# Performance work log

Hardware: AMD Instinct MI355X
Metric: run time of the kernel (lower is better)

The kernel has to match this reference:

```python
import jax, jax.numpy as jnp
import numpy as np

V, E, H, T = 50000, 512, 256, 32  # vocab, embed dim, per-direction hidden, tagset
START, STOP = 30, 31
S = 2048  # sequence length
NEG = -10000.0


def setup_inputs() -> dict:
    key = jax.random.key(0)
    ks = jax.random.split(key, 16)
    sentence = jax.random.randint(ks[0], (S,), 0, V)
    embed = jax.random.normal(ks[1], (V, E), dtype=jnp.float32)
    # PyTorch LSTM layout: gates stacked [i, f, g, o], each H rows
    w_ih_f = jax.random.normal(ks[2], (4 * H, E), dtype=jnp.float32) * 0.05
    w_hh_f = jax.random.normal(ks[3], (4 * H, H), dtype=jnp.float32) * 0.05
    b_f = jax.random.normal(ks[4], (4 * H,), dtype=jnp.float32) * 0.05  # b_ih + b_hh fused
    w_ih_b = jax.random.normal(ks[5], (4 * H, E), dtype=jnp.float32) * 0.05
    w_hh_b = jax.random.normal(ks[6], (4 * H, H), dtype=jnp.float32) * 0.05
    b_b = jax.random.normal(ks[7], (4 * H,), dtype=jnp.float32) * 0.05
    w_tag = jax.random.normal(ks[8], (T, 2 * H), dtype=jnp.float32) * 0.05
    b_tag = jax.random.normal(ks[9], (T,), dtype=jnp.float32) * 0.05
    transitions = jax.random.normal(ks[10], (T, T), dtype=jnp.float32)
    transitions = transitions.at[START, :].set(NEG)  # nothing transitions into START
    transitions = transitions.at[:, STOP].set(NEG)   # nothing transitions out of STOP
    h0 = jax.random.normal(ks[11], (2, H), dtype=jnp.float32)  # [fwd/bwd, H]
    c0 = jax.random.normal(ks[12], (2, H), dtype=jnp.float32)
    return {"sentence": sentence, "embed": embed, "w_ih_f": w_ih_f, "w_hh_f": w_hh_f,
            "b_f": b_f, "w_ih_b": w_ih_b, "w_hh_b": w_hh_b, "b_b": b_b,
            "w_tag": w_tag, "b_tag": b_tag, "transitions": transitions,
            "h0": h0, "c0": c0}


def _run_lstm(x, w_ih, w_hh, b, h, c):
    # x: [S, E]; precompute input projections for all steps at once
    px = x @ w_ih.T + b  # [S, 4H]

    def step(carry, p):
        h, c = carry
        g = p + h @ w_hh.T  # [4H]
        i, f, gg, o = jnp.split(g, 4)
        c = jax.nn.sigmoid(f) * c + jax.nn.sigmoid(i) * jnp.tanh(gg)
        h = jax.nn.sigmoid(o) * jnp.tanh(c)
        return (h, c), h

    _, hs = jax.lax.scan(step, (h, c), px)
    return hs  # [S, H]


def _lstm_features(sentence, embed, w_ih_f, w_hh_f, b_f, w_ih_b, w_hh_b, b_b,
                   w_tag, b_tag, h0, c0):
    emb = embed[sentence]  # [S, E]
    h_fwd = _run_lstm(emb, w_ih_f, w_hh_f, b_f, h0[0], c0[0])
    h_bwd = _run_lstm(emb[::-1], w_ih_b, w_hh_b, b_b, h0[1], c0[1])[::-1]
    hs = jnp.concatenate([h_fwd, h_bwd], axis=-1)  # [S, 2H]
    return hs @ w_tag.T + b_tag  # [S, T]


def _viterbi(feats, transitions):
    init = jnp.full((T,), NEG, dtype=feats.dtype).at[START].set(0.0)

    def step(fv, feat):
        scores = fv[None, :] + transitions  # [next_tag, prev_tag]
        bptrs = jnp.argmax(scores, axis=1)  # [T]
        fv_new = jnp.max(scores, axis=1) + feat
        return fv_new, bptrs

    fv, bptrs = jax.lax.scan(step, init, feats)  # bptrs: [S, T]
    terminal = fv + transitions[STOP]
    best_last = jnp.argmax(terminal)
    path_score = terminal[best_last]

    def back(tag, bp):
        return bp[tag], tag

    _, tag_seq = jax.lax.scan(back, best_last, bptrs, reverse=True)  # [S]
    return path_score, tag_seq


def reference(sentence, embed, w_ih_f, w_hh_f, b_f, w_ih_b, w_hh_b, b_b,
              w_tag, b_tag, transitions, h0, c0):
    feats = _lstm_features(sentence, embed, w_ih_f, w_hh_f, b_f,
                           w_ih_b, w_hh_b, b_b, w_tag, b_tag, h0, c0)
    score, tag_seq = _viterbi(feats, transitions)
    return score, tag_seq
```

## Files before the change

kernel.cpp:

```cpp
#include <hip/hip_runtime.h>
#include <cstdint>
#include <cmath>

constexpr int SEQ  = 2048;
constexpr int EMB  = 512;
constexpr int HID  = 256;
constexpr int GATE = 1024;
constexpr int NTAG = 32;
constexpr float FNEG = -10000.0f;
constexpr int DBLK = 8;

__global__ __launch_bounds__(256) void px_gemm(
    const int* __restrict__ sent, const float* __restrict__ embed,
    const float* __restrict__ w_ih_f, const float* __restrict__ b_f,
    const float* __restrict__ w_ih_b, const float* __restrict__ b_b,
    float* __restrict__ px)
{
  const int dir = blockIdx.z;
  const int tm = blockIdx.x, tn = blockIdx.y;
  const float* __restrict__ w_ih = dir ? w_ih_b : w_ih_f;
  const float* __restrict__ bias = dir ? b_b : b_f;
  __shared__ float As[64][65];
  __shared__ float Bs[64][65];
  __shared__ int sidx[64];
  const int tid = threadIdx.x;
  if (tid < 64) {
    const int s = tm * 64 + tid;
    const int tpos = dir ? (SEQ - 1 - s) : s;
    sidx[tid] = sent[tpos];
  }
  __syncthreads();
  float acc[4][4] = {};
  const int tr = tid >> 4, tc = tid & 15;
  for (int k0 = 0; k0 < EMB; k0 += 64) {
    #pragma unroll
    for (int i = 0; i < 4; ++i) {
      const int v = tid + i * 256;
      const int r = v >> 4, kv = v & 15;
      const float4 a4 = *reinterpret_cast<const float4*>(
          &embed[(size_t)sidx[r] * EMB + k0 + kv * 4]);
      As[r][kv*4+0] = a4.x; As[r][kv*4+1] = a4.y;
      As[r][kv*4+2] = a4.z; As[r][kv*4+3] = a4.w;
      const float4 b4 = *reinterpret_cast<const float4*>(
          &w_ih[(size_t)(tn * 64 + r) * EMB + k0 + kv * 4]);
      Bs[r][kv*4+0] = b4.x; Bs[r][kv*4+1] = b4.y;
      Bs[r][kv*4+2] = b4.z; Bs[r][kv*4+3] = b4.w;
    }
    __syncthreads();
    #pragma unroll
    for (int kk = 0; kk < 64; ++kk) {
      float a[4], b[4];
      #pragma unroll
      for (int i = 0; i < 4; ++i) a[i] = As[tr + 16 * i][kk];
      #pragma unroll
      for (int jj = 0; jj < 4; ++jj) b[jj] = Bs[tc + 16 * jj][kk];
      #pragma unroll
      for (int i = 0; i < 4; ++i)
        #pragma unroll
        for (int jj = 0; jj < 4; ++jj)
          acc[i][jj] = fmaf(a[i], b[jj], acc[i][jj]);
    }
    __syncthreads();
  }
  #pragma unroll
  for (int i = 0; i < 4; ++i) {
    const int srow = tm * 64 + tr + 16 * i;
    #pragma unroll
    for (int jj = 0; jj < 4; ++jj) {
      const int j = tn * 64 + tc + 16 * jj;
      px[((size_t)dir * SEQ + srow) * GATE + j] = acc[i][jj] + bias[j];
    }
  }
}

__global__ __attribute__((amdgpu_flat_work_group_size(256, 256),
                          amdgpu_waves_per_eu(1, 1)))
void lstm_sync(
    const float* __restrict__ px, const float* __restrict__ w_hh_f,
    const float* __restrict__ w_hh_b, const float* __restrict__ h0,
    const float* __restrict__ c0, float* __restrict__ hs,
    unsigned long long* __restrict__ hx)
{
  const int blk = blockIdx.x;
  const int dir = blk >> 3, b = blk & 7;
  const int tid = threadIdx.x;
  const int j = tid >> 3;
  const int q = tid & 7;
  const int u = 32 * b + j;
  const float* __restrict__ w_hh = dir ? w_hh_b : w_hh_f;

  float4 wi[8], wf[8], wg[8], wo[8];
  {
    const float* __restrict__ r0 = &w_hh[(size_t)u * HID + 32 * q];
    const float* __restrict__ r1 = r0 + (size_t)256 * HID;
    const float* __restrict__ r2 = r0 + (size_t)512 * HID;
    const float* __restrict__ r3 = r0 + (size_t)768 * HID;
    #pragma unroll
    for (int m = 0; m < 8; ++m) {
      wi[m] = *reinterpret_cast<const float4*>(&r0[4 * m]);
      wf[m] = *reinterpret_cast<const float4*>(&r1[4 * m]);
      wg[m] = *reinterpret_cast<const float4*>(&r2[4 * m]);
      wo[m] = *reinterpret_cast<const float4*>(&r3[4 * m]);
    }
  }
  #pragma unroll
  for (int m = 0; m < 8; ++m) {
    asm volatile(""
      : "+v"(wi[m].x), "+v"(wi[m].y), "+v"(wi[m].z), "+v"(wi[m].w),
        "+v"(wf[m].x), "+v"(wf[m].y), "+v"(wf[m].z), "+v"(wf[m].w),
        "+v"(wg[m].x), "+v"(wg[m].y), "+v"(wg[m].z), "+v"(wg[m].w),
        "+v"(wo[m].x), "+v"(wo[m].y), "+v"(wo[m].z), "+v"(wo[m].w));
  }

  __shared__ float hsh[2][8 * 36];
  float c = 0.0f;
  hsh[0][36 * (tid >> 5) + (tid & 31)] = h0[dir * HID + tid];
  if (q == 0) c = c0[dir * HID + u];
  __syncthreads();

  const size_t pxbase = (size_t)dir * SEQ * GATE;
  float pi = 0.f, pf = 0.f, pg = 0.f, po = 0.f;
  if (q == 0) {
    pi = px[pxbase + u];        pf = px[pxbase + 256 + u];
    pg = px[pxbase + 512 + u];  po = px[pxbase + 768 + u];
  }

  for (int t = 0; t < SEQ; ++t) {
    const float* __restrict__ hb = hsh[t & 1];
    float*       __restrict__ nb = hsh[(t & 1) ^ 1];

    float ni = 0.f, nf = 0.f, ng = 0.f, no = 0.f;
    if (q == 0 && t + 1 < SEQ) {
      const size_t nbx = pxbase + (size_t)(t + 1) * GATE;
      ni = px[nbx + u];        nf = px[nbx + 256 + u];
      ng = px[nbx + 512 + u];  no = px[nbx + 768 + u];
    }

    float si = 0.f, sf = 0.f, sg = 0.f, so = 0.f;
    #pragma unroll
    for (int m = 0; m < 8; ++m) {
      const float4 h4 = *reinterpret_cast<const float4*>(&hb[36 * q + 4 * m]);
      si = fmaf(h4.x, wi[m].x, si); si = fmaf(h4.y, wi[m].y, si);
      si = fmaf(h4.z, wi[m].z, si); si = fmaf(h4.w, wi[m].w, si);
      sf = fmaf(h4.x, wf[m].x, sf); sf = fmaf(h4.y, wf[m].y, sf);
      sf = fmaf(h4.z, wf[m].z, sf); sf = fmaf(h4.w, wf[m].w, sf);
      sg = fmaf(h4.x, wg[m].x, sg); sg = fmaf(h4.y, wg[m].y, sg);
      sg = fmaf(h4.z, wg[m].z, sg); sg = fmaf(h4.w, wg[m].w, sg);
      so = fmaf(h4.x, wo[m].x, so); so = fmaf(h4.y, wo[m].y, so);
      so = fmaf(h4.z, wo[m].z, so); so = fmaf(h4.w, wo[m].w, so);
    }
    #pragma unroll
    for (int off = 4; off >= 1; off >>= 1) {
      si += __shfl_down(si, off, 8);
      sf += __shfl_down(sf, off, 8);
      sg += __shfl_down(sg, off, 8);
      so += __shfl_down(so, off, 8);
    }

    if (q == 0) {
      const float gi = si + pi, gf = sf + pf, gg = sg + pg, go = so + po;
      const float ai = 1.0f / (1.0f + expf(-gi));
      const float af = 1.0f / (1.0f + expf(-gf));
      const float ao = 1.0f / (1.0f + expf(-go));
      c = af * c + ai * tanhf(gg);
      const float hn = ao * tanhf(c);
      const unsigned long long pk =
          ((unsigned long long)(unsigned)(t + 1) << 32) |
          (unsigned long long)__float_as_uint(hn);
      __hip_atomic_store(&hx[((size_t)dir * SEQ + t) * HID + u], pk,
                         __ATOMIC_RELAXED, __HIP_MEMORY_SCOPE_AGENT);
      nb[36 * b + j] = hn;
      hs[((size_t)dir * SEQ + t) * HID + u] = hn;
    }
    pi = ni; pf = nf; pg = ng; po = no;
    if (t == SEQ - 1) break;

    {
      const size_t gidx = ((size_t)dir * SEQ + t) * HID + tid;
      const unsigned want = (unsigned)(t + 1);
      bool need = (tid >> 5) != b;
      while (true) {
        if (need) {
          const unsigned long long v = __hip_atomic_load(
              &hx[gidx], __ATOMIC_RELAXED, __HIP_MEMORY_SCOPE_AGENT);
          if ((unsigned)(v >> 32) == want) {
            nb[36 * (tid >> 5) + (tid & 31)] = __uint_as_float((unsigned)v);
            need = false;
          }
        }
        if (__ballot(need) == 0ULL) break;
        __builtin_amdgcn_s_sleep(1);
      }
    }
    __syncthreads();
  }
}

__global__ __launch_bounds__(256) void feats_kernel(
    const float* __restrict__ hs, const float* __restrict__ w_tag,
    const float* __restrict__ b_tag, float* __restrict__ feats)
{
  const int t = blockIdx.x;
  const int tid = threadIdx.x;
  const int j = tid >> 3, p = tid & 7;
  const float* __restrict__ src = (p < 4)
      ? (hs + (size_t)t * HID + p * 64)
      : (hs + (size_t)(SEQ + (SEQ - 1 - t)) * HID + (p - 4) * 64);
  const float* __restrict__ wt = w_tag + (size_t)j * (2 * HID) + p * 64;
  float sum = 0.f;
  #pragma unroll
  for (int k = 0; k < 64; k += 4) {
    const float4 x4 = *reinterpret_cast<const float4*>(&src[k]);
    const float4 w4 = *reinterpret_cast<const float4*>(&wt[k]);
    sum = fmaf(x4.x, w4.x, sum); sum = fmaf(x4.y, w4.y, sum);
    sum = fmaf(x4.z, w4.z, sum); sum = fmaf(x4.w, w4.w, sum);
  }
  sum += __shfl_down(sum, 4, 8);
  sum += __shfl_down(sum, 2, 8);
  sum += __shfl_down(sum, 1, 8);
  if (p == 0) feats[(size_t)t * NTAG + j] = sum + b_tag[j];
}

__global__ __launch_bounds__(64) void viterbi_kernel(
    const float* __restrict__ feats, const float* __restrict__ trans,
    float* __restrict__ out)
{
  __shared__ unsigned char bp[SEQ][NTAG];
  const int lane = threadIdx.x;
  const int j = lane & 31, half = lane >> 5;
  float tr[16];
  #pragma unroll
  for (int qq = 0; qq < 16; ++qq) tr[qq] = trans[j * NTAG + half * 16 + qq];
  float fv = (j == 30) ? 0.0f : FNEG;
  float fcur = feats[j];
  for (int t = 0; t < SEQ; ++t) {
    const int tn = (t + 1 < SEQ) ? (t + 1) : (SEQ - 1);
    const float fnext = feats[(size_t)tn * NTAG + j];
    float best = -3.0e38f; int barg = 0;
    #pragma unroll
    for (int qq = 0; qq < 16; ++qq) {
      const int p = half * 16 + qq;
      const float sc = __shfl(fv, p) + tr[qq];
      if (sc > best) { best = sc; barg = p; }
    }
    const float ob = __shfl_down(best, 32);
    const int   oa = __shfl_down(barg, 32);
    float fvnew = 0.f;
    if (half == 0) {
      if (ob > best) { best = ob; barg = oa; }
      bp[t][j] = (unsigned char)barg;
      fvnew = best + fcur;
    }
    fv = __shfl(fvnew, j);
    fcur = fnext;
  }
  float term = fv + trans[31 * NTAG + j];
  int idx = j;
  #pragma unroll
  for (int off = 16; off >= 1; off >>= 1) {
    const float ov = __shfl_down(term, off, 32);
    const int   oi = __shfl_down(idx, off, 32);
    if (ov > term) { term = ov; idx = oi; }
  }
  if (lane == 0) {
    out[0] = term;
    int tag = idx;
    for (int t = SEQ - 1; t >= 0; --t) {
      out[1 + t] = (float)tag;
      tag = bp[t][tag];
    }
  }
}

extern "C" void kernel_launch(void* const* d_in, const int* in_sizes, int n_in,
                              void* d_out, int out_size, void* d_ws, size_t ws_size,
                              hipStream_t stream)
{
  (void)in_sizes; (void)n_in; (void)out_size; (void)ws_size;
  const int*   sent   = (const int*)  d_in[0];
  const float* embed  = (const float*)d_in[1];
  const float* w_ih_f = (const float*)d_in[2];
  const float* w_hh_f = (const float*)d_in[3];
  const float* b_f    = (const float*)d_in[4];
  const float* w_ih_b = (const float*)d_in[5];
  const float* w_hh_b = (const float*)d_in[6];
  const float* b_b    = (const float*)d_in[7];
  const float* w_tag  = (const float*)d_in[8];
  const float* b_tag  = (const float*)d_in[9];
  const float* trans  = (const float*)d_in[10];
  const float* h0     = (const float*)d_in[11];
  const float* c0     = (const float*)d_in[12];
  float* out = (float*)d_out;

  unsigned long long* hx = (unsigned long long*)d_ws;
  float* px    = (float*)(hx + (size_t)2 * SEQ * HID);
  float* hsbuf = px + (size_t)2 * SEQ * GATE;
  float* feats = hsbuf + (size_t)2 * SEQ * HID;

  dim3 gemm_grid(SEQ / 64, GATE / 64, 2);
  px_gemm<<<gemm_grid, 256, 0, stream>>>(sent, embed, w_ih_f, b_f,
                                         w_ih_b, b_b, px);
  lstm_sync<<<2 * DBLK, 256, 0, stream>>>(px, w_hh_f, w_hh_b, h0, c0,
                                          hsbuf, hx);
  feats_kernel<<<SEQ, 256, 0, stream>>>(hsbuf, w_tag, b_tag, feats);
  viterbi_kernel<<<1, 64, 0, stream>>>(feats, trans, out);
}
```

Measured before the change: 6.210 ms.

## Co-locate LSTM recurrence blocks on one XCD and poll via L2-coherent loads

Launches 128 blocks, reads each block's XCD id from a hardware register, and chooses the XCD with the most resident blocks. The first 16 blocks that landed there run the recurrence and the rest exit, so all cross-block h exchange stays within one XCD's L2. The spin loop polls with sc0 loads, which are L2-coherent within that XCD, and falls back to sc0 sc1 system-coherent loads after many failed rounds. It also stops sleeping for the first few rounds to cut exchange latency. The main risks are that the chosen XCD may hold fewer than 16 blocks, which would stall or break the run, and the extra control kernel and startup handshake.

```diff
diff --git a/kernel.cpp b/kernel.cpp
--- a/kernel.cpp
+++ b/kernel.cpp
@@ -8,7 +8,8 @@
 constexpr int GATE = 1024;
 constexpr int NTAG = 32;
 constexpr float FNEG = -10000.0f;
-constexpr int DBLK = 8;
+constexpr int NBLK = 128;
+constexpr int NWORK = 16;
 
 __global__ __launch_bounds__(256) void px_gemm(
     const int* __restrict__ sent, const float* __restrict__ embed,
@@ -73,17 +74,70 @@
   }
 }
 
+__global__ void init_ctl(unsigned* ctl) {
+  if (threadIdx.x < 16) ctl[threadIdx.x] = 0u;
+}
+
+__device__ __forceinline__ unsigned long long ld_l2(
+    const unsigned long long* p) {
+  unsigned long long v;
+  asm volatile("global_load_dwordx2 %0, %1, off sc0\n\ts_waitcnt vmcnt(0)"
+               : "=v"(v) : "v"(p) : "memory");
+  return v;
+}
+__device__ __forceinline__ unsigned long long ld_llc(
+    const unsigned long long* p) {
+  unsigned long long v;
+  asm volatile("global_load_dwordx2 %0, %1, off sc0 sc1\n\ts_waitcnt vmcnt(0)"
+               : "=v"(v) : "v"(p) : "memory");
+  return v;
+}
+
 __global__ __attribute__((amdgpu_flat_work_group_size(256, 256),
                           amdgpu_waves_per_eu(1, 1)))
-void lstm_sync(
+void lstm_xcd(
     const float* __restrict__ px, const float* __restrict__ w_hh_f,
     const float* __restrict__ w_hh_b, const float* __restrict__ h0,
     const float* __restrict__ c0, float* __restrict__ hs,
-    unsigned long long* __restrict__ hx)
-{
-  const int blk = blockIdx.x;
-  const int dir = blk >> 3, b = blk & 7;
+    unsigned long long* __restrict__ hx, unsigned* __restrict__ ctl)
+{
   const int tid = threadIdx.x;
+  __shared__ int s_asn;
+  if (tid == 0) {
+    unsigned xcd = __builtin_amdgcn_s_getreg(63508) & 7u;
+    atomicAdd(&ctl[1 + xcd], 1u);
+    __threadfence();
+    atomicAdd(&ctl[0], 1u);
+    if (blockIdx.x == 0) {
+      while (__hip_atomic_load(&ctl[0], __ATOMIC_RELAXED,
+                               __HIP_MEMORY_SCOPE_AGENT) < (unsigned)NBLK)
+        __builtin_amdgcn_s_sleep(16);
+      __threadfence();
+      unsigned best = 0, bc = 0;
+      for (unsigned x = 0; x < 8; ++x) {
+        const unsigned cx = __hip_atomic_load(&ctl[1 + x], __ATOMIC_RELAXED,
+                                              __HIP_MEMORY_SCOPE_AGENT);
+        if (cx > bc) { bc = cx; best = x; }
+      }
+      __hip_atomic_store(&ctl[9], 0x100u | best, __ATOMIC_RELAXED,
+                         __HIP_MEMORY_SCOPE_AGENT);
+    }
+    unsigned ch;
+    while (((ch = __hip_atomic_load(&ctl[9], __ATOMIC_RELAXED,
+                                    __HIP_MEMORY_SCOPE_AGENT)) & 0x100u) == 0)
+      __builtin_amdgcn_s_sleep(16);
+    int mine = -1;
+    if ((ch & 7u) == xcd) {
+      const unsigned idx = atomicAdd(&ctl[10], 1u);
+      if (idx < (unsigned)NWORK) mine = (int)idx;
+    }
+    s_asn = mine;
+  }
+  __syncthreads();
+  const int asn = s_asn;
+  if (asn < 0) return;
+  const int dir = asn >> 3, b = asn & 7;
+
   const int j = tid >> 3;
   const int q = tid & 7;
   const int u = 32 * b + j;
@@ -125,6 +179,7 @@
     pg = px[pxbase + 512 + u];  po = px[pxbase + 768 + u];
   }
 
+  bool fast = true;
   for (int t = 0; t < SEQ; ++t) {
     const float* __restrict__ hb = hsh[t & 1];
     float*       __restrict__ nb = hsh[(t & 1) ^ 1];
@@ -176,20 +231,22 @@
     if (t == SEQ - 1) break;
 
     {
-      const size_t gidx = ((size_t)dir * SEQ + t) * HID + tid;
+      const unsigned long long* pp = &hx[((size_t)dir * SEQ + t) * HID + tid];
       const unsigned want = (unsigned)(t + 1);
       bool need = (tid >> 5) != b;
+      int rounds = 0;
       while (true) {
         if (need) {
-          const unsigned long long v = __hip_atomic_load(
-              &hx[gidx], __ATOMIC_RELAXED, __HIP_MEMORY_SCOPE_AGENT);
+          const unsigned long long v = fast ? ld_l2(pp) : ld_llc(pp);
           if ((unsigned)(v >> 32) == want) {
             nb[36 * (tid >> 5) + (tid & 31)] = __uint_as_float((unsigned)v);
             need = false;
           }
         }
         if (__ballot(need) == 0ULL) break;
-        __builtin_amdgcn_s_sleep(1);
+        ++rounds;
+        if (rounds > 200) fast = false;
+        if (rounds > 4) __builtin_amdgcn_s_sleep(1);
       }
     }
     __syncthreads();
@@ -296,12 +353,14 @@
   float* px    = (float*)(hx + (size_t)2 * SEQ * HID);
   float* hsbuf = px + (size_t)2 * SEQ * GATE;
   float* feats = hsbuf + (size_t)2 * SEQ * HID;
-
+  unsigned* ctl = (unsigned*)(feats + (size_t)SEQ * NTAG);
+
+  init_ctl<<<1, 64, 0, stream>>>(ctl);
   dim3 gemm_grid(SEQ / 64, GATE / 64, 2);
   px_gemm<<<gemm_grid, 256, 0, stream>>>(sent, embed, w_ih_f, b_f,
                                          w_ih_b, b_b, px);
-  lstm_sync<<<2 * DBLK, 256, 0, stream>>>(px, w_hh_f, w_hh_b, h0, c0,
-                                          hsbuf, hx);
+  lstm_xcd<<<NBLK, 256, 0, stream>>>(px, w_hh_f, w_hh_b, h0, c0,
+                                     hsbuf, hx, ctl);
   feats_kernel<<<SEQ, 256, 0, stream>>>(hsbuf, w_tag, b_tag, feats);
   viterbi_kernel<<<1, 64, 0, stream>>>(feats, trans, out);
 }
```

After: 5.485 ms. -11.7%, faster.
